# Optimization experiments

Hardware: AMD Instinct MI355X
Metric: run time of the kernel (lower is better)

The kernel has to match this reference:

```python
import jax, jax.numpy as jnp
import numpy as np

N_NODES = 100000
N_EDGES = 3200000
IN_C, HID_C, OUT_C = 64, 64, 32


def setup_inputs() -> dict:
    key = jax.random.key(0)
    ks = jax.random.split(key, 8)
    x = jax.random.normal(ks[0], (N_NODES, IN_C), dtype=jnp.float32)
    edge_index = jax.random.randint(ks[1], (2, N_EDGES), 0, N_NODES, dtype=jnp.int64)
    s1 = 1.0 / np.sqrt(IN_C)
    s2 = 1.0 / np.sqrt(HID_C)
    W1l = jax.random.uniform(ks[2], (IN_C, HID_C), jnp.float32, -s1, s1)
    b1l = jnp.zeros((HID_C,), jnp.float32)
    W1r = jax.random.uniform(ks[3], (IN_C, HID_C), jnp.float32, -s1, s1)
    W2l = jax.random.uniform(ks[4], (HID_C, OUT_C), jnp.float32, -s2, s2)
    b2l = jnp.zeros((OUT_C,), jnp.float32)
    W2r = jax.random.uniform(ks[5], (HID_C, OUT_C), jnp.float32, -s2, s2)
    return {"x": x, "edge_index": edge_index, "W1l": W1l, "b1l": b1l,
            "W1r": W1r, "W2l": W2l, "b2l": b2l, "W2r": W2r}


def _sage_conv(x, src, dst, Wl, bl, Wr):
    # mean-aggregate source features onto destination nodes
    msg = x[src]                                              # [E, d] gather
    summed = jax.ops.segment_sum(msg, dst, num_segments=N_NODES)
    deg = jax.ops.segment_sum(jnp.ones((src.shape[0],), x.dtype), dst,
                              num_segments=N_NODES)
    agg = summed / jnp.maximum(deg, 1.0)[:, None]             # [N, d]
    return agg @ Wl + bl + x @ Wr                             # lin_l(agg)+lin_r(x)


def reference(x, edge_index, W1l, b1l, W1r, W2l, b2l, W2r):
    src, dst = edge_index[0], edge_index[1]
    h = jax.nn.relu(_sage_conv(x, src, dst, W1l, b1l, W1r))
    # dropout is identity in eval mode
    return _sage_conv(h, src, dst, W2l, b2l, W2r)
```

## Files before the change

### kernel.cpp

```cpp
#include <hip/hip_runtime.h>
#include <hip/hip_bf16.h>

#define N_NODES 100000
#define N_EDGES 3200000
#define NBKT 391
#define BKT_CAP 10240

typedef __hip_bfloat16 bf16;
typedef unsigned int uint;
typedef __attribute__((ext_vector_type(8))) short bf16x8;
typedef __attribute__((ext_vector_type(4))) float f32x4;

__device__ __forceinline__ float b2f(bf16 v) { return __bfloat162float(v); }

__device__ __forceinline__ float bits2f(unsigned short w) {
    union { unsigned short u; bf16 b; } c;
    c.u = w;
    return __bfloat162float(c.b);
}
__device__ __forceinline__ unsigned short f2bits(float f) {
    return (unsigned short)(__float_as_uint(f) >> 16);
}
__device__ __forceinline__ unsigned short f2bf_bits(float f) {
    bf16 b = __float2bfloat16(f);
    unsigned short u;
    __builtin_memcpy(&u, &b, 2);
    return u;
}
__device__ __forceinline__ float lo16f(uint w) { return __uint_as_float(w << 16); }
__device__ __forceinline__ float hi16f(uint w) { return __uint_as_float(w & 0xffff0000u); }

__device__ __forceinline__ int get_idx(const void* ei, long long pos, int is64) {
    if (is64) return (int)((const long long*)ei)[pos];
    return ((const int*)ei)[pos];
}
__device__ __forceinline__ float get_f(const void* p, long long pos, int isbf) {
    if (isbf) return b2f(((const bf16*)p)[pos]);
    return ((const float*)p)[pos];
}

__global__ void detect_kernel(const void* __restrict__ x,
                              const void* __restrict__ ei,
                              int* __restrict__ flags) {
    int lane = threadIdx.x;
    const unsigned short* xw = (const unsigned short*)x;
    float v = bits2f(xw[2 * lane]);
    bool plaus = (v == v) && fabsf(v) > 1e-3f && fabsf(v) < 1e2f;
    unsigned long long m1 = __ballot(plaus);
    const int* iw = (const int*)ei;
    bool z = (iw[2 * lane + 1] == 0);
    unsigned long long m2 = __ballot(z);
    if (lane == 0) {
        flags[0] = (__popcll(m1) >= 32) ? 1 : 0;
        flags[1] = (__popcll(m2) == 64) ? 1 : 0;
    }
}

__global__ __launch_bounds__(256) void transpose_kernel(
    const void* __restrict__ x, uint4* __restrict__ xt,
    const int* __restrict__ flags) {
    if (!flags[0]) return;
    int i = blockIdx.x * 256 + threadIdx.x;
    if (i >= N_NODES * 4) return;
    int node = i >> 2, cz = i & 3;
    const uint4* x4 = (const uint4*)x;
    uint4 a = x4[(long long)node * 8 + cz * 2];
    uint4 b = x4[(long long)node * 8 + cz * 2 + 1];
    long long o = (long long)cz * (N_NODES * 2) + (long long)node * 2;
    xt[o] = a;
    xt[o + 1] = b;
}

__global__ __launch_bounds__(256) void scatterA_kernel(
    const void* __restrict__ ei, int* __restrict__ bucket_cursor,
    uint* __restrict__ bucket_data, const int* __restrict__ flags) {
    __shared__ int lhist[NBKT];
    __shared__ int lbase[NBKT];
    int is64 = flags[1];
    int t = threadIdx.x;
    int chunk0 = blockIdx.x * 8192;
    int dreg[32];

    for (int i = t; i < NBKT; i += 256) lhist[i] = 0;
    __syncthreads();
#pragma unroll
    for (int j = 0; j < 32; j++) {
        int e = chunk0 + j * 256 + t;
        int d = -1;
        if (e < N_EDGES) {
            d = get_idx(ei, (long long)N_EDGES + e, is64);
            atomicAdd(&lhist[d >> 8], 1);
        }
        dreg[j] = d;
    }
    __syncthreads();
    for (int i = t; i < NBKT; i += 256) {
        int c = lhist[i];
        lbase[i] = c ? atomicAdd(&bucket_cursor[i], c) : 0;
        lhist[i] = 0;
    }
    __syncthreads();
#pragma unroll
    for (int j = 0; j < 32; j++) {
        int e = chunk0 + j * 256 + t;
        int d = dreg[j];
        if (d >= 0) {
            int s = get_idx(ei, e, is64);
            int b = d >> 8;
            int o = lbase[b] + atomicAdd(&lhist[b], 1);
            if (o < BKT_CAP)
                bucket_data[(long long)b * BKT_CAP + o] = ((uint)(d & 255) << 17) | (uint)s;
        }
    }
}

__global__ void scanBuckets_kernel(const int* __restrict__ cnt,
                                   int* __restrict__ base) {
    __shared__ int buf[512];
    int t = threadIdx.x;
    int v = (t < NBKT) ? cnt[t] : 0;
    buf[t] = v;
    __syncthreads();
    for (int off = 1; off < 512; off <<= 1) {
        int add = (t >= off) ? buf[t - off] : 0;
        __syncthreads();
        buf[t] += add;
        __syncthreads();
    }
    if (t < NBKT) base[t] = buf[t] - v;
}

__global__ __launch_bounds__(256) void csrB_kernel(
    const int* __restrict__ bucket_cnt, const int* __restrict__ bucket_base,
    const uint* __restrict__ bucket_data, int* __restrict__ csr_src,
    int* __restrict__ row_start) {
    __shared__ int lh[256];
    __shared__ int buf[256];
    int b = blockIdx.x;
    int t = threadIdx.x;
    int cnt = bucket_cnt[b];
    if (cnt > BKT_CAP) cnt = BKT_CAP;
    int base = bucket_base[b];
    const uint* bd = bucket_data + (long long)b * BKT_CAP;

    lh[t] = 0;
    __syncthreads();
    for (int i = t; i < cnt; i += 256) atomicAdd(&lh[bd[i] >> 17], 1);
    __syncthreads();
    int v = lh[t];
    buf[t] = v;
    __syncthreads();
    for (int off = 1; off < 256; off <<= 1) {
        int add = (t >= off) ? buf[t - off] : 0;
        __syncthreads();
        buf[t] += add;
        __syncthreads();
    }
    int excl = buf[t] - v;
    int g = (b << 8) + t;
    if (g < N_NODES) row_start[g] = base + excl;
    lh[t] = excl;
    __syncthreads();
    for (int i = t; i < cnt; i += 256) {
        uint e = bd[i];
        int o = atomicAdd(&lh[e >> 17], 1);
        csr_src[base + o] = (int)(e & 0x1FFFFu);
    }
    if (b == 0 && t == 0) row_start[N_NODES] = N_EDGES;
}

#define ACCF4(acc, v, v2)                                                        \
    acc[0] += __uint_as_float((v).x) + __uint_as_float((v2).x);                   \
    acc[1] += __uint_as_float((v).y) + __uint_as_float((v2).y);                   \
    acc[2] += __uint_as_float((v).z) + __uint_as_float((v2).z);                   \
    acc[3] += __uint_as_float((v).w) + __uint_as_float((v2).w);

__device__ __forceinline__ void slice_gather8(
    const uint* __restrict__ su, const int* __restrict__ row_start,
    const int* __restrict__ csr_src, int nb0, int g8, int c8, int lane,
    float& a0, float& a1, int& dg_out) {
    int rl = (lane <= 8) ? row_start[nb0 + lane] : 0;
    int sg = __shfl(rl, g8 >> 3, 64);
    int eg = __shfl(rl, (g8 >> 3) + 1, 64);
    int dg = eg - sg;
    int maxd = dg;
    maxd = max(maxd, __shfl_xor(maxd, 8, 64));
    maxd = max(maxd, __shfl_xor(maxd, 16, 64));
    maxd = max(maxd, __shfl_xor(maxd, 32, 64));

    float s0f = 0.0f, s1f = 0.0f;
    for (int base = 0; base < maxd; base += 8) {
        int pf = sg + base + c8;
        int sreg = (pf < eg) ? csr_src[pf] : 0;
#pragma unroll
        for (int u = 0; u < 8; u += 4) {
            int s0 = __shfl(sreg, g8 + u, 64);
            int s1 = __shfl(sreg, g8 + u + 1, 64);
            int s2 = __shfl(sreg, g8 + u + 2, 64);
            int s3 = __shfl(sreg, g8 + u + 3, 64);
            uint w0 = 0, w1 = 0, w2 = 0, w3 = 0;
            if (base + u < dg)     w0 = su[(s0 << 3) + c8];
            if (base + u + 1 < dg) w1 = su[(s1 << 3) + c8];
            if (base + u + 2 < dg) w2 = su[(s2 << 3) + c8];
            if (base + u + 3 < dg) w3 = su[(s3 << 3) + c8];
            s0f += lo16f(w0) + lo16f(w1) + lo16f(w2) + lo16f(w3);
            s1f += hi16f(w0) + hi16f(w1) + hi16f(w2) + hi16f(w3);
        }
    }
    a0 = s0f;
    a1 = s1f;
    dg_out = dg;
}

__global__ __launch_bounds__(256) void gather1_kernel(
    const void* __restrict__ x, const uint* __restrict__ xtu,
    const int* __restrict__ row_start, const int* __restrict__ csr_src,
    bf16* __restrict__ aggbuf, const int* __restrict__ flags) {
    int isbf = flags[0];
    int t = threadIdx.x;
    int lane = t & 63;
    int w = t >> 6;
    int bid = blockIdx.x;

    if (isbf) {
        int cz = (bid & 7) >> 1;
        int wid = ((((bid >> 3) << 1) | (bid & 1)) << 2) + w;
        int nw = gridDim.x;
        int g8 = lane & 0x38, c8 = lane & 7;
        int g = lane >> 3;
        const uint* su = xtu + (long long)cz * (N_NODES * 8);
        uint* ag = (uint*)aggbuf;
        for (int oct = wid; oct < N_NODES / 8; oct += nw) {
            int nb0 = oct * 8;
            float a0, a1;
            int dg;
            slice_gather8(su, row_start, csr_src, nb0, g8, c8, lane, a0, a1, dg);
            float inv = 1.0f / fmaxf((float)dg, 1.0f);
            uint pk = (uint)f2bf_bits(a0 * inv) | ((uint)f2bf_bits(a1 * inv) << 16);
            ag[(nb0 + g) * 32 + cz * 8 + c8] = pk;
        }
    } else {
        int gw = (bid * 256 + t) >> 6;
        int nwv = (gridDim.x * 256) >> 6;
        int e4 = lane >> 4, q16 = lane & 15;
        const uint4* xf = (const uint4*)x;
        for (int p = gw; p * 2 < N_NODES; p += nwv) {
            int na = p * 2, nb = p * 2 + 1;
            int sa = row_start[na], ea = row_start[na + 1];
            int sb = row_start[nb], eb = row_start[nb + 1];
            int da = ea - sa, db = eb - sb;
            int maxd = max(da, db);
            float accA[4] = {0, 0, 0, 0};
            float accB[4] = {0, 0, 0, 0};
            for (int off = 0; off < maxd; off += 16) {
                int iA0 = sa + off + e4, iA1 = iA0 + 4, iA2 = iA0 + 8, iA3 = iA0 + 12;
                int iB0 = sb + off + e4, iB1 = iB0 + 4, iB2 = iB0 + 8, iB3 = iB0 + 12;
                int sA0 = (iA0 < ea) ? csr_src[iA0] : -1;
                int sA1 = (iA1 < ea) ? csr_src[iA1] : -1;
                int sA2 = (iA2 < ea) ? csr_src[iA2] : -1;
                int sA3 = (iA3 < ea) ? csr_src[iA3] : -1;
                int sB0 = (iB0 < eb) ? csr_src[iB0] : -1;
                int sB1 = (iB1 < eb) ? csr_src[iB1] : -1;
                int sB2 = (iB2 < eb) ? csr_src[iB2] : -1;
                int sB3 = (iB3 < eb) ? csr_src[iB3] : -1;
                uint4 vA0 = {0,0,0,0}, vA1 = {0,0,0,0}, vA2 = {0,0,0,0}, vA3 = {0,0,0,0};
                uint4 vB0 = {0,0,0,0}, vB1 = {0,0,0,0}, vB2 = {0,0,0,0}, vB3 = {0,0,0,0};
                if (sA0 >= 0) vA0 = xf[sA0 * 16 + q16];
                if (sA1 >= 0) vA1 = xf[sA1 * 16 + q16];
                if (sA2 >= 0) vA2 = xf[sA2 * 16 + q16];
                if (sA3 >= 0) vA3 = xf[sA3 * 16 + q16];
                if (sB0 >= 0) vB0 = xf[sB0 * 16 + q16];
                if (sB1 >= 0) vB1 = xf[sB1 * 16 + q16];
                if (sB2 >= 0) vB2 = xf[sB2 * 16 + q16];
                if (sB3 >= 0) vB3 = xf[sB3 * 16 + q16];
                ACCF4(accA, vA0, vA1)
                ACCF4(accA, vA2, vA3)
                ACCF4(accB, vB0, vB1)
                ACCF4(accB, vB2, vB3)
            }
#pragma unroll
            for (int m = 16; m <= 32; m <<= 1)
#pragma unroll
                for (int k = 0; k < 4; k++) {
                    accA[k] += __shfl_xor(accA[k], m, 64);
                    accB[k] += __shfl_xor(accB[k], m, 64);
                }
            float avA = 0.0f, avB = 0.0f;
#pragma unroll
            for (int k = 0; k < 4; k++) {
                float vA = __shfl(accA[k], lane >> 2, 64);
                float vB = __shfl(accB[k], lane >> 2, 64);
                avA = ((lane & 3) == k) ? vA : avA;
                avB = ((lane & 3) == k) ? vB : avB;
            }
            avA *= 1.0f / fmaxf((float)da, 1.0f);
            avB *= 1.0f / fmaxf((float)db, 1.0f);
            aggbuf[(long long)na * 64 + lane] = __float2bfloat16(avA);
            aggbuf[(long long)nb * 64 + lane] = __float2bfloat16(avB);
        }
    }
}

__global__ __launch_bounds__(256) void gemm1_kernel(
    const void* __restrict__ x, const bf16* __restrict__ aggbuf,
    const void* __restrict__ W1l, const void* __restrict__ b1l,
    const void* __restrict__ W1r, const void* __restrict__ W2l,
    const void* __restrict__ b2l, const void* __restrict__ W2r,
    bf16* __restrict__ zbufT, bf16* __restrict__ rbufT,
    const int* __restrict__ flags) {
    __shared__ __align__(16) unsigned short sW1t[64][136];
    __shared__ __align__(16) unsigned short sA[64][136];
    __shared__ __align__(16) unsigned short sW2t[64][72];
    __shared__ __align__(16) unsigned short sH[64][72];
    __shared__ float sB1[64];
    __shared__ float sB2[32];

    int isbf = flags[0];
    int t = threadIdx.x;
    int n0 = blockIdx.x * 64;

    for (int i = t; i < 64 * 128; i += 256) {
        int n = i & 63, k = i >> 6;
        unsigned short v;
        if (isbf)
            v = (k < 64) ? ((const unsigned short*)W1l)[k * 64 + n]
                         : ((const unsigned short*)W1r)[(k - 64) * 64 + n];
        else
            v = f2bits((k < 64) ? ((const float*)W1l)[k * 64 + n]
                                : ((const float*)W1r)[(k - 64) * 64 + n]);
        sW1t[n][k] = v;
    }
    for (int i = t; i < 64 * 64; i += 256) {
        int n = i & 63, k = i >> 6;
        unsigned short v;
        if (isbf)
            v = (n < 32) ? ((const unsigned short*)W2l)[k * 32 + n]
                         : ((const unsigned short*)W2r)[k * 32 + (n - 32)];
        else
            v = f2bits((n < 32) ? ((const float*)W2l)[k * 32 + n]
                                : ((const float*)W2r)[k * 32 + (n - 32)]);
        sW2t[n][k] = v;
    }
    if (t < 64) sB1[t] = get_f(b1l, t, isbf);
    if (t < 32) sB2[t] = get_f(b2l, t, isbf);

    const uint4* ag4 = (const uint4*)aggbuf;
    if (isbf) {
        const uint4* x4 = (const uint4*)x;
        for (int i = t; i < 64 * 16; i += 256) {
            int m = i >> 4, c = i & 15;
            int nn = min(n0 + m, N_NODES - 1);
            uint4 v = (c < 8) ? ag4[(long long)nn * 8 + c]
                              : x4[(long long)nn * 8 + (c - 8)];
            *(uint4*)&sA[m][c * 8] = v;
        }
    } else {
        for (int i = t; i < 64 * 8; i += 256) {
            int m = i >> 3, c = i & 7;
            int nn = min(n0 + m, N_NODES - 1);
            *(uint4*)&sA[m][c * 8] = ag4[(long long)nn * 8 + c];
        }
        const float* xf = (const float*)x;
        for (int i = t; i < 64 * 64; i += 256) {
            int m = i >> 6, c = i & 63;
            int nn = min(n0 + m, N_NODES - 1);
            sA[m][64 + c] = f2bf_bits(xf[(long long)nn * 64 + c]);
        }
    }
    __syncthreads();

    int w = t >> 6, lane = t & 63;
    int mbase = w * 16;
    int q = lane >> 4, r15 = lane & 15;
    f32x4 acc1[4] = {{0,0,0,0},{0,0,0,0},{0,0,0,0},{0,0,0,0}};
#pragma unroll
    for (int ks = 0; ks < 4; ks++) {
        bf16x8 afrag = *(const bf16x8*)&sA[mbase + r15][ks * 32 + q * 8];
#pragma unroll
        for (int nt = 0; nt < 4; nt++) {
            bf16x8 bfrag = *(const bf16x8*)&sW1t[nt * 16 + r15][ks * 32 + q * 8];
            acc1[nt] = __builtin_amdgcn_mfma_f32_16x16x32_bf16(afrag, bfrag, acc1[nt], 0, 0, 0);
        }
    }
#pragma unroll
    for (int nt = 0; nt < 4; nt++) {
        int col = nt * 16 + r15;
        float bias = sB1[col];
#pragma unroll
        for (int rr = 0; rr < 4; rr++) {
            int m = mbase + q * 4 + rr;
            sH[m][col] = f2bf_bits(fmaxf(acc1[nt][rr] + bias, 0.0f));
        }
    }
    __syncthreads();

    f32x4 acc2[4] = {{0,0,0,0},{0,0,0,0},{0,0,0,0},{0,0,0,0}};
#pragma unroll
    for (int ks = 0; ks < 2; ks++) {
        bf16x8 afrag = *(const bf16x8*)&sH[mbase + r15][ks * 32 + q * 8];
#pragma unroll
        for (int nt = 0; nt < 4; nt++) {
            bf16x8 bfrag = *(const bf16x8*)&sW2t[nt * 16 + r15][ks * 32 + q * 8];
            acc2[nt] = __builtin_amdgcn_mfma_f32_16x16x32_bf16(afrag, bfrag, acc2[nt], 0, 0, 0);
        }
    }
#pragma unroll
    for (int nt = 0; nt < 4; nt++) {
        int col = nt * 16 + r15;
#pragma unroll
        for (int rr = 0; rr < 4; rr++) {
            int m = mbase + q * 4 + rr;
            int n = n0 + m;
            if (n < N_NODES) {
                float v = acc2[nt][rr];
                if (col < 32) {
                    zbufT[(long long)(col >> 4) * (N_NODES * 16) +
                          (long long)n * 16 + (col & 15)] = __float2bfloat16(v);
                } else {
                    int c2 = col - 32;
                    rbufT[(long long)(c2 >> 4) * (N_NODES * 16) +
                          (long long)n * 16 + (c2 & 15)] =
                        __float2bfloat16(v + sB2[c2]);
                }
            }
        }
    }
}

__global__ __launch_bounds__(256) void node2_kernel(
    const int* __restrict__ row_start, const int* __restrict__ csr_src,
    const uint* __restrict__ zTu, const bf16* __restrict__ rbufT,
    void* __restrict__ out, const int* __restrict__ flags) {
    int isbf = flags[0];
    int t = threadIdx.x;
    int lane = t & 63;
    int w = t >> 6;
    int bid = blockIdx.x;
    int cz = (bid & 7) >> 2;
    int wid = ((((bid >> 3) << 2) | (bid & 3)) << 2) + w;
    int nw = gridDim.x * 2;
    int g8 = lane & 0x38, c8 = lane & 7;
    int g = lane >> 3;
    const uint* su = zTu + (long long)cz * (N_NODES * 8);
    const uint* ru = (const uint*)(rbufT + (long long)cz * (N_NODES * 16));

    for (int oct = wid; oct < N_NODES / 8; oct += nw) {
        int nb0 = oct * 8;
        float a0, a1;
        int dg;
        slice_gather8(su, row_start, csr_src, nb0, g8, c8, lane, a0, a1, dg);
        float inv = 1.0f / fmaxf((float)dg, 1.0f);
        int n = nb0 + g;
        uint rb = ru[n * 8 + c8];
        float r0 = a0 * inv + lo16f(rb);
        float r1 = a1 * inv + hi16f(rb);
        if (isbf) {
            uint pk = (uint)f2bf_bits(r0) | ((uint)f2bf_bits(r1) << 16);
            ((uint*)out)[n * 16 + cz * 8 + c8] = pk;
        } else {
            ((float*)out)[(long long)n * 32 + cz * 16 + 2 * c8] = r0;
            ((float*)out)[(long long)n * 32 + cz * 16 + 2 * c8 + 1] = r1;
        }
    }
}

extern "C" void kernel_launch(void* const* d_in, const int* in_sizes, int n_in,
                              void* d_out, int out_size, void* d_ws, size_t ws_size,
                              hipStream_t stream) {
    const void* x = d_in[0];
    const void* ei = d_in[1];
    const void* W1l = d_in[2];
    const void* b1l = d_in[3];
    const void* W1r = d_in[4];
    const void* W2l = d_in[5];
    const void* b2l = d_in[6];
    const void* W2r = d_in[7];

    char* ws = (char*)d_ws;
    uint* bucket_data = (uint*)ws;
    bf16* aggbuf = (bf16*)ws;
    int* csr_src = (int*)(ws + 16015424);
    int* row_start = (int*)(ws + 28815424);
    int* bucket_cursor = (int*)(ws + 29215488);
    int* bucket_base = (int*)(ws + 29217088);
    uint* xtu = (uint*)(ws + 29218688);
    bf16* zbufT = (bf16*)(ws + 29218688);
    bf16* rbufT = (bf16*)(ws + 35618688);
    int* flags = (int*)(ws + 42018688);

    hipMemsetAsync(bucket_cursor, 0, NBKT * 4, stream);

    detect_kernel<<<1, 64, 0, stream>>>(x, ei, flags);
    transpose_kernel<<<1563, 256, 0, stream>>>(x, (uint4*)xtu, flags);
    scatterA_kernel<<<NBKT, 256, 0, stream>>>(ei, bucket_cursor, bucket_data, flags);
    scanBuckets_kernel<<<1, 512, 0, stream>>>(bucket_cursor, bucket_base);
    csrB_kernel<<<NBKT, 256, 0, stream>>>(bucket_cursor, bucket_base, bucket_data,
                                          csr_src, row_start);
    gather1_kernel<<<4096, 256, 0, stream>>>(x, xtu, row_start, csr_src, aggbuf,
                                             flags);
    gemm1_kernel<<<1563, 256, 0, stream>>>(x, aggbuf, W1l, b1l, W1r, W2l, b2l,
                                           W2r, zbufT, rbufT, flags);
    node2_kernel<<<4096, 256, 0, stream>>>(row_start, csr_src, (const uint*)zbufT,
                                           rbufT, d_out, flags);
}
```

Before: 374.4 us.

## Use XCD-aware dynamic work stealing for layer-1 gather slices

The layer-1 gather no longer assigns channel slices and node octets statically by block id. Each wavefront reads its XCD id from a hardware register, starts on the channel slice tied to that XCD pair, and pulls octets from a per-slice atomic cursor. After its own slice is exhausted it moves on to the other slices. The intent is to balance uneven per-node degree work while keeping each XCD's L2 focused on one slice of the transposed features. The cost is one atomic per octet and a fragile assumption about hardware register 20's layout, and a gcursor memset is added to the launch sequence.

```diff
diff --git a/kernel.cpp b/kernel.cpp
--- a/kernel.cpp
+++ b/kernel.cpp
@@ -5,6 +5,7 @@
 #define N_EDGES 3200000
 #define NBKT 391
 #define BKT_CAP 10240
+#define NOCT (N_NODES / 8)
 
 typedef __hip_bfloat16 bf16;
 typedef unsigned int uint;
@@ -29,6 +30,12 @@
 }
 __device__ __forceinline__ float lo16f(uint w) { return __uint_as_float(w << 16); }
 __device__ __forceinline__ float hi16f(uint w) { return __uint_as_float(w & 0xffff0000u); }
+
+__device__ __forceinline__ int get_xcd() {
+    uint v;
+    asm volatile("s_getreg_b32 %0, hwreg(20, 0, 32)" : "=s"(v));
+    return (int)(v & 7);
+}
 
 __device__ __forceinline__ int get_idx(const void* ei, long long pos, int is64) {
     if (is64) return (int)((const long long*)ei)[pos];
@@ -215,29 +222,36 @@
 __global__ __launch_bounds__(256) void gather1_kernel(
     const void* __restrict__ x, const uint* __restrict__ xtu,
     const int* __restrict__ row_start, const int* __restrict__ csr_src,
-    bf16* __restrict__ aggbuf, const int* __restrict__ flags) {
+    bf16* __restrict__ aggbuf, int* __restrict__ gcursor,
+    const int* __restrict__ flags) {
     int isbf = flags[0];
     int t = threadIdx.x;
     int lane = t & 63;
-    int w = t >> 6;
     int bid = blockIdx.x;
 
     if (isbf) {
-        int cz = (bid & 7) >> 1;
-        int wid = ((((bid >> 3) << 1) | (bid & 1)) << 2) + w;
-        int nw = gridDim.x;
         int g8 = lane & 0x38, c8 = lane & 7;
         int g = lane >> 3;
-        const uint* su = xtu + (long long)cz * (N_NODES * 8);
+        int cz0 = (get_xcd() >> 1) & 3;
         uint* ag = (uint*)aggbuf;
-        for (int oct = wid; oct < N_NODES / 8; oct += nw) {
-            int nb0 = oct * 8;
-            float a0, a1;
-            int dg;
-            slice_gather8(su, row_start, csr_src, nb0, g8, c8, lane, a0, a1, dg);
-            float inv = 1.0f / fmaxf((float)dg, 1.0f);
-            uint pk = (uint)f2bf_bits(a0 * inv) | ((uint)f2bf_bits(a1 * inv) << 16);
-            ag[(nb0 + g) * 32 + cz * 8 + c8] = pk;
+        for (int k = 0; k < 4; k++) {
+            int cz = (cz0 + k) & 3;
+            const uint* su = xtu + (long long)cz * (N_NODES * 8);
+            while (true) {
+                int oct = 0;
+                if (lane == 0) oct = atomicAdd(&gcursor[cz], 1);
+                oct = __shfl(oct, 0, 64);
+                if (oct >= NOCT) break;
+                int nb0 = oct * 8;
+                float a0, a1;
+                int dg;
+                slice_gather8(su, row_start, csr_src, nb0, g8, c8, lane,
+                              a0, a1, dg);
+                float inv = 1.0f / fmaxf((float)dg, 1.0f);
+                uint pk = (uint)f2bf_bits(a0 * inv) |
+                          ((uint)f2bf_bits(a1 * inv) << 16);
+                ag[(nb0 + g) * 32 + cz * 8 + c8] = pk;
+            }
         }
     } else {
         int gw = (bid * 256 + t) >> 6;
@@ -444,7 +458,7 @@
     const uint* su = zTu + (long long)cz * (N_NODES * 8);
     const uint* ru = (const uint*)(rbufT + (long long)cz * (N_NODES * 16));
 
-    for (int oct = wid; oct < N_NODES / 8; oct += nw) {
+    for (int oct = wid; oct < NOCT; oct += nw) {
         int nb0 = oct * 8;
         float a0, a1;
         int dg;
@@ -487,8 +501,10 @@
     bf16* zbufT = (bf16*)(ws + 29218688);
     bf16* rbufT = (bf16*)(ws + 35618688);
     int* flags = (int*)(ws + 42018688);
+    int* gcursor = (int*)(ws + 42018696);
 
     hipMemsetAsync(bucket_cursor, 0, NBKT * 4, stream);
+    hipMemsetAsync(gcursor, 0, 16, stream);
 
     detect_kernel<<<1, 64, 0, stream>>>(x, ei, flags);
     transpose_kernel<<<1563, 256, 0, stream>>>(x, (uint4*)xtu, flags);
@@ -497,7 +513,7 @@
     csrB_kernel<<<NBKT, 256, 0, stream>>>(bucket_cursor, bucket_base, bucket_data,
                                           csr_src, row_start);
     gather1_kernel<<<4096, 256, 0, stream>>>(x, xtu, row_start, csr_src, aggbuf,
-                                             flags);
+                                             gcursor, flags);
     gemm1_kernel<<<1563, 256, 0, stream>>>(x, aggbuf, W1l, b1l, W1r, W2l, b2l,
                                            W2r, zbufT, rbufT, flags);
     node2_kernel<<<4096, 256, 0, stream>>>(row_start, csr_src, (const uint*)zbufT,
```

Result: faster. 366.1 us (-2.2%).
